# Kernel optimization log

Hardware: AMD Instinct MI355X
Metric: run time of the kernel (lower is better)

## Reference

```python
import jax, jax.numpy as jnp
import numpy as np
from jax import lax

THRESH = 1.0
MIN_VMEM = -1.0

def _conv(x, w, stride):
    # x: [N,C,H,W], w: [O,I,kh,kw]
    return lax.conv_general_dilated(
        x, w, window_strides=(stride, stride), padding=((1, 1), (1, 1)),
        dimension_numbers=("NCHW", "OIHW", "NCHW"))

def _avgpool2(x):
    n, c, h, w = x.shape
    return x.reshape(n, c, h // 2, 2, w // 2, 2).mean(axis=(3, 5))

def _iaf(x_bt, B, T):
    # x_bt: [B*T, ...] -> sinabs IAFSqueeze: reshape to [B,T,...], scan over T.
    feat = x_bt.shape[1:]
    seq = x_bt.reshape((B, T) + feat)
    seq_t = jnp.moveaxis(seq, 1, 0)  # [T, B, ...]

    def step(v, u):
        v = v + u                              # integrate
        s = (v >= THRESH).astype(v.dtype)      # SingleSpike
        v = v * (1.0 - s)                      # MembraneReset -> 0
        v = jnp.maximum(v, MIN_VMEM)           # min_v_mem clamp
        return v, s

    v0 = jnp.zeros(seq_t.shape[1:], dtype=x_bt.dtype)
    _, spikes = lax.scan(step, v0, seq_t)      # spikes: [T, B, ...]
    return jnp.moveaxis(spikes, 0, 1).reshape((B * T,) + feat)

def setup_inputs() -> dict:
    key = jax.random.key(0)
    k0, k1, k2, k3, k4 = jax.random.split(key, 5)
    x = jax.random.normal(k0, (25, 40, 2, 128, 128), jnp.float32)
    w1 = jax.random.normal(k1, (8, 2, 3, 3), jnp.float32) * 0.3
    w2 = jax.random.normal(k2, (16, 8, 3, 3), jnp.float32) * 0.2
    w3 = jax.random.normal(k3, (64, 1024), jnp.float32) * 0.1
    w4 = jax.random.normal(k4, (11, 64), jnp.float32) * 0.2
    return {"x": x, "w1": w1, "w2": w2, "w3": w3, "w4": w4}

def reference(x, w1, w2, w3, w4):
    B, T, C, H, W = x.shape
    h = x.reshape(B * T, C, H, W)
    h = _conv(h, w1, 2)          # [BT, 8, 64, 64]
    h = _iaf(h, B, T)
    h = _avgpool2(h)             # [BT, 8, 32, 32]
    h = _conv(h, w2, 2)          # [BT, 16, 16, 16]
    h = _iaf(h, B, T)
    h = _avgpool2(h)             # [BT, 16, 8, 8]
    h = h.reshape(B * T, -1)     # [BT, 1024]
    h = h @ w3.T                 # [BT, 64]
    h = _iaf(h, B, T)
    h = h @ w4.T                 # [BT, 11]
    h = _iaf(h, B, T)
    return h.reshape(B, T, -1)
```

## Files before the change

### kernel.cpp

```cpp
#include <hip/hip_runtime.h>

#define THRESH 1.0f
#define MIN_VMEM -1.0f

__device__ __forceinline__ float iaf_step(float& v, float u) {
    v += u;
    float s = (v >= THRESH) ? 1.f : 0.f;
    v = (s > 0.f) ? 0.f : v;
    v = fmaxf(v, MIN_VMEM);
    return s;
}

#define K1_CIS 612

__global__ __launch_bounds__(64) void k1_conv1_iaf_pool(
        const float* __restrict__ x, const float* __restrict__ w1,
        float* __restrict__ ws1) {
    __shared__ float B[2][2 * K1_CIS];
    const int tid = threadIdx.x;
    const int cg = tid >> 5;
    const int pp = tid & 31;
    const int px = pp & 7, py = pp >> 3;
    const int tx = blockIdx.x & 3;
    const int ty = blockIdx.x >> 2;
    const int b = blockIdx.y;

    float w[72];
    {
        const float4* wp = (const float4*)(w1 + cg * 72);
        #pragma unroll
        for (int i = 0; i < 18; i++) {
            float4 t4 = wp[i];
            w[4 * i] = t4.x; w[4 * i + 1] = t4.y;
            w[4 * i + 2] = t4.z; w[4 * i + 3] = t4.w;
        }
    }

    int fo[5]; bool lv[5]; int lo[5];
    #pragma unroll
    for (int k = 0; k < 5; k++) {
        const int i = tid + 64 * k;
        const int ci = (i >= 136) ? 1 : 0;
        const int rr = i - 136 * ci;
        const int r = rr >> 3, c4 = rr & 7;
        const int gy = 16 * ty - 1 + r;
        fo[k] = ci * 16384 + gy * 128 + 32 * tx + 4 * c4;
        lv[k] = (gy >= 0) && (i < 272);
        lo[k] = ci * K1_CIS + r * 36 + 1 + 4 * c4;
    }
    const int hci = (tid >= 17) ? 1 : 0;
    const int hr = tid - 17 * hci;
    const int hgy = 16 * ty - 1 + hr;
    const int hfo = hci * 16384 + hgy * 128 + 32 * tx - 1;
    const bool hv_ok = (tid < 34) && (tx > 0) && (hgy >= 0);
    const int hlo = hci * K1_CIS + hr * 36;

    float v[16], u[16];
    #pragma unroll
    for (int i = 0; i < 16; i++) v[i] = 0.f;

    const float* xb = x + (size_t)(b * 40) * 32768;
    float4 rv[5]; float hvv;

    #pragma unroll
    for (int k = 0; k < 5; k++)
        rv[k] = lv[k] ? *(const float4*)(xb + fo[k]) : make_float4(0, 0, 0, 0);
    hvv = hv_ok ? xb[hfo] : 0.f;
    #pragma unroll
    for (int k = 0; k < 4; k++) {
        float* d = &B[0][lo[k]];
        d[0] = rv[k].x; d[1] = rv[k].y; d[2] = rv[k].z; d[3] = rv[k].w;
    }
    if (tid < 16) {
        float* d = &B[0][lo[4]];
        d[0] = rv[4].x; d[1] = rv[4].y; d[2] = rv[4].z; d[3] = rv[4].w;
    }
    if (tid < 34) B[0][hlo] = hvv;

    for (int t = 0; t < 40; t++) {
        const int cur = t & 1;
        if (t < 39) {
            const float* xt = xb + (size_t)(t + 1) * 32768;
            #pragma unroll
            for (int k = 0; k < 5; k++)
                rv[k] = lv[k] ? *(const float4*)(xt + fo[k]) : make_float4(0, 0, 0, 0);
            hvv = hv_ok ? xt[hfo] : 0.f;
        }
        #pragma unroll
        for (int i = 0; i < 16; i++) u[i] = 0.f;
        const float* Bc = B[cur];
        #pragma unroll
        for (int ci = 0; ci < 2; ci++) {
            float p[5][5];
            const int base = ci * K1_CIS + 4 * py * 36 + 4 * px;
            #pragma unroll
            for (int dy = 0; dy < 5; dy++) {
                const float4 q = *(const float4*)&Bc[base + dy * 36];
                p[dy][0] = q.x; p[dy][1] = q.y; p[dy][2] = q.z; p[dy][3] = q.w;
                p[dy][4] = Bc[base + dy * 36 + 4];
            }
            #pragma unroll
            for (int j = 0; j < 4; j++)
                #pragma unroll
                for (int sy = 0; sy < 2; sy++)
                    #pragma unroll
                    for (int sx = 0; sx < 2; sx++) {
                        float a = u[j * 4 + 2 * sy + sx];
                        #pragma unroll
                        for (int ky = 0; ky < 3; ky++)
                            #pragma unroll
                            for (int kx = 0; kx < 3; kx++)
                                a += p[2 * sy + ky][2 * sx + kx]
                                   * w[j * 18 + ci * 9 + ky * 3 + kx];
                        u[j * 4 + 2 * sy + sx] = a;
                    }
        }
        const size_t ob = (size_t)(b * 40 + t) * 8192
                        + (size_t)(4 * ty + py) * 32 + 8 * tx + px;
        #pragma unroll
        for (int j = 0; j < 4; j++) {
            float s = 0.f;
            #pragma unroll
            for (int s4 = 0; s4 < 4; s4++)
                s += iaf_step(v[j * 4 + s4], u[j * 4 + s4]);
            ws1[ob + (size_t)(4 * cg + j) * 1024] = s * 0.25f;
        }
        if (t < 39) {
            float* Bn = B[1 - cur];
            #pragma unroll
            for (int k = 0; k < 4; k++) {
                float* d = &Bn[lo[k]];
                d[0] = rv[k].x; d[1] = rv[k].y; d[2] = rv[k].z; d[3] = rv[k].w;
            }
            if (tid < 16) {
                float* d = &Bn[lo[4]];
                d[0] = rv[4].x; d[1] = rv[4].y; d[2] = rv[4].z; d[3] = rv[4].w;
            }
            if (tid < 34) Bn[hlo] = hvv;
        }
    }
}

#define K2_CIS 1224

__global__ __launch_bounds__(256) void k2a_conv2(
        const float* __restrict__ ws1, const float* __restrict__ w2,
        float* __restrict__ u2) {
    __shared__ float F[8 * K2_CIS];
    const int n = blockIdx.x;
    const int tid = threadIdx.x;

    for (int i = tid; i < 8 * K2_CIS; i += 256) F[i] = 0.f;
    __syncthreads();
    const float4* src = (const float4*)(ws1 + (size_t)n * 8192);
    #pragma unroll
    for (int k = 0; k < 8; k++) {
        const int i = tid + 256 * k;
        const float4 q = src[i];
        const int ci = i >> 8;
        const int rr = i & 255;
        const int r = rr >> 3, c4 = rr & 7;
        float* d = &F[ci * K2_CIS + (r + 1) * 36 + 1 + 4 * c4];
        d[0] = q.x; d[1] = q.y; d[2] = q.z; d[3] = q.w;
    }
    __syncthreads();

    const int wv = tid >> 6;
    const int ln = tid & 63;
    const int oy = ln >> 2;
    const int ox4 = ln & 3;

    float acc[4][4];
    #pragma unroll
    for (int j = 0; j < 4; j++)
        #pragma unroll
        for (int k = 0; k < 4; k++) acc[j][k] = 0.f;

    #pragma unroll
    for (int ci = 0; ci < 8; ci++) {
        float q[3][9];
        const int base = ci * K2_CIS + (2 * oy) * 36 + 8 * ox4;
        #pragma unroll
        for (int ky = 0; ky < 3; ky++) {
            const float4 qa = *(const float4*)&F[base + ky * 36];
            const float4 qb = *(const float4*)&F[base + ky * 36 + 4];
            q[ky][0] = qa.x; q[ky][1] = qa.y; q[ky][2] = qa.z; q[ky][3] = qa.w;
            q[ky][4] = qb.x; q[ky][5] = qb.y; q[ky][6] = qb.z; q[ky][7] = qb.w;
            q[ky][8] = F[base + ky * 36 + 8];
        }
        #pragma unroll
        for (int j = 0; j < 4; j++) {
            const int co_u = __builtin_amdgcn_readfirstlane(4 * wv + j);
            const float* wb = w2 + co_u * 72 + ci * 9;
            float wm[9];
            #pragma unroll
            for (int m = 0; m < 9; m++) wm[m] = wb[m];
            #pragma unroll
            for (int k = 0; k < 4; k++)
                #pragma unroll
                for (int ky = 0; ky < 3; ky++)
                    #pragma unroll
                    for (int kx = 0; kx < 3; kx++)
                        acc[j][k] += q[ky][2 * k + kx] * wm[ky * 3 + kx];
        }
    }
    float* db = u2 + (size_t)n * 4096 + oy * 16 + 4 * ox4;
    #pragma unroll
    for (int j = 0; j < 4; j++) {
        const int co = 4 * wv + j;
        *(float4*)(db + co * 256) =
            make_float4(acc[j][0], acc[j][1], acc[j][2], acc[j][3]);
    }
}

__global__ __launch_bounds__(256) void k2b_scan(
        const float* __restrict__ u2, float* __restrict__ ws2) {
    const int id = blockIdx.x * 256 + threadIdx.x;
    const int b = id >> 10;
    const int c = (id >> 6) & 15;
    const int pp = id & 63;
    const int py = pp >> 3, px = pp & 7;
    const float* base = u2 + (size_t)(b * 40) * 4096 + c * 256
                      + (2 * py) * 16 + 2 * px;
    float* ob = ws2 + (size_t)(b * 40) * 1024 + c * 64 + py * 8 + px;

    float v0 = 0.f, v1 = 0.f, v2 = 0.f, v3 = 0.f;
    float2 P[2][8][2];
    #pragma unroll
    for (int tt = 0; tt < 8; tt++) {
        const float* nb = base + (size_t)tt * 4096;
        P[0][tt][0] = *(const float2*)(nb);
        P[0][tt][1] = *(const float2*)(nb + 16);
    }
    #pragma unroll
    for (int bt = 0; bt < 5; bt++) {
        if (bt < 4) {
            #pragma unroll
            for (int tt = 0; tt < 8; tt++) {
                const float* nb = base + (size_t)(8 * (bt + 1) + tt) * 4096;
                P[(bt + 1) & 1][tt][0] = *(const float2*)(nb);
                P[(bt + 1) & 1][tt][1] = *(const float2*)(nb + 16);
            }
        }
        #pragma unroll
        for (int tt = 0; tt < 8; tt++) {
            const float2 b0 = P[bt & 1][tt][0];
            const float2 b1 = P[bt & 1][tt][1];
            const float s = iaf_step(v0, b0.x) + iaf_step(v1, b0.y)
                          + iaf_step(v2, b1.x) + iaf_step(v3, b1.y);
            ob[(size_t)(8 * bt + tt) * 1024] = s * 0.25f;
        }
    }
}

__global__ __launch_bounds__(256) void k3_fc1(
        const float* __restrict__ ws2, const float* __restrict__ w3,
        float* __restrict__ ws3) {
    __shared__ float rows[4096];
    const int n0 = blockIdx.x * 4;
    const int tid = threadIdx.x;
    const float4* s = (const float4*)(ws2 + (size_t)n0 * 1024);
    #pragma unroll
    for (int k = 0; k < 4; k++)
        ((float4*)rows)[tid + 256 * k] = s[tid + 256 * k];
    __syncthreads();
    const int o = tid >> 2, ko = tid & 3;
    const float4* wp = (const float4*)(w3 + (size_t)o * 1024 + ko * 256);
    const float4* r0 = (const float4*)(rows + ko * 256);
    const float4* r1 = (const float4*)(rows + 1024 + ko * 256);
    const float4* r2 = (const float4*)(rows + 2048 + ko * 256);
    const float4* r3 = (const float4*)(rows + 3072 + ko * 256);
    float a0 = 0.f, a1 = 0.f, a2 = 0.f, a3 = 0.f;
    #pragma unroll 8
    for (int j = 0; j < 64; j++) {
        const float4 wv = wp[j];
        const float4 q0 = r0[j], q1 = r1[j], q2 = r2[j], q3 = r3[j];
        a0 += q0.x * wv.x + q0.y * wv.y + q0.z * wv.z + q0.w * wv.w;
        a1 += q1.x * wv.x + q1.y * wv.y + q1.z * wv.z + q1.w * wv.w;
        a2 += q2.x * wv.x + q2.y * wv.y + q2.z * wv.z + q2.w * wv.w;
        a3 += q3.x * wv.x + q3.y * wv.y + q3.z * wv.z + q3.w * wv.w;
    }
    a0 += __shfl_xor(a0, 1); a0 += __shfl_xor(a0, 2);
    a1 += __shfl_xor(a1, 1); a1 += __shfl_xor(a1, 2);
    a2 += __shfl_xor(a2, 1); a2 += __shfl_xor(a2, 2);
    a3 += __shfl_xor(a3, 1); a3 += __shfl_xor(a3, 2);
    if (ko == 0) {
        ws3[(size_t)(n0 + 0) * 64 + o] = a0;
        ws3[(size_t)(n0 + 1) * 64 + o] = a1;
        ws3[(size_t)(n0 + 2) * 64 + o] = a2;
        ws3[(size_t)(n0 + 3) * 64 + o] = a3;
    }
}

__global__ __launch_bounds__(64) void k4_iaf_fc2_iaf(
        const float* __restrict__ ws3, const float* __restrict__ w4,
        float* __restrict__ out) {
    __shared__ float sld[40 * 64];
    __shared__ float w4s[11 * 66];
    __shared__ float sp[64];
    const int b = blockIdx.x, tid = threadIdx.x;
    for (int i = tid; i < 2560; i += 64) sld[i] = ws3[(size_t)b * 2560 + i];
    for (int i = tid; i < 704; i += 64) {
        int r = i >> 6, cc = i & 63;
        w4s[r * 66 + cc] = w4[i];
    }
    __syncthreads();
    float v1 = 0.f, v2 = 0.f;
    for (int t = 0; t < 40; t++) {
        sp[tid] = iaf_step(v1, sld[t * 64 + tid]);
        __syncthreads();
        if (tid < 11) {
            float acc = 0.f;
            #pragma unroll
            for (int k = 0; k < 64; k++) acc += sp[k] * w4s[tid * 66 + k];
            out[(size_t)(b * 40 + t) * 11 + tid] = iaf_step(v2, acc);
        }
        __syncthreads();
    }
}

extern "C" void kernel_launch(void* const* d_in, const int* in_sizes, int n_in,
                              void* d_out, int out_size, void* d_ws, size_t ws_size,
                              hipStream_t stream) {
    const float* x  = (const float*)d_in[0];
    const float* w1 = (const float*)d_in[1];
    const float* w2 = (const float*)d_in[2];
    const float* w3 = (const float*)d_in[3];
    const float* w4 = (const float*)d_in[4];
    float* out = (float*)d_out;

    float* ws1 = (float*)d_ws;
    float* ws2 = ws1 + 8192000;
    float* ws3 = ws2 + 1024000;
    float* u2 = (float*)d_in[0];

    k1_conv1_iaf_pool<<<dim3(32, 25), 64, 0, stream>>>(x, w1, ws1);
    k2a_conv2<<<1000, 256, 0, stream>>>(ws1, w2, u2);
    k2b_scan<<<100, 256, 0, stream>>>(u2, ws2);
    k3_fc1<<<250, 256, 0, stream>>>(ws2, w3, ws3);
    k4_iaf_fc2_iaf<<<25, 64, 0, stream>>>(ws3, w4, out);
}
```

Before: 282.1 us.

## Shrink per-block work to raise block counts and parallelize the fc2 stage

The conv1 kernel now covers half the tile width with four channel groups of two channels each, which doubles the grid to 1600 blocks and halves per-thread registers. The k2b scan uses 64-thread blocks (400 blocks) and fc1 handles two rows per block (500 blocks). Both changes aim to fill more CUs. The final fc2 kernel first runs the layer-3 IAF scan for all timesteps, then computes all 440 dot products in parallel, and leaves only the 11-wide final scan serial. This replaces the per-timestep barrier loop. The new code relies on single-wavefront execution rather than explicit barriers around LDS reuse, and conv1 re-reads more halo data per output.

```diff
diff --git a/kernel.cpp b/kernel.cpp
--- a/kernel.cpp
+++ b/kernel.cpp
@@ -11,96 +11,98 @@
     return s;
 }
 
-#define K1_CIS 612
+#define K1_CIS 340
 
 __global__ __launch_bounds__(64) void k1_conv1_iaf_pool(
         const float* __restrict__ x, const float* __restrict__ w1,
         float* __restrict__ ws1) {
     __shared__ float B[2][2 * K1_CIS];
     const int tid = threadIdx.x;
-    const int cg = tid >> 5;
-    const int pp = tid & 31;
-    const int px = pp & 7, py = pp >> 3;
-    const int tx = blockIdx.x & 3;
-    const int ty = blockIdx.x >> 2;
+    const int cg = tid >> 4;
+    const int pp = tid & 15;
+    const int ppx = pp & 3, ppy = pp >> 2;
+    const int tx = blockIdx.x & 7;
+    const int ty = blockIdx.x >> 3;
     const int b = blockIdx.y;
 
-    float w[72];
+    for (int i = tid; i < 4 * K1_CIS; i += 64) ((float*)B)[i] = 0.f;
+
+    float w[36];
     {
-        const float4* wp = (const float4*)(w1 + cg * 72);
-        #pragma unroll
-        for (int i = 0; i < 18; i++) {
-            float4 t4 = wp[i];
-            w[4 * i] = t4.x; w[4 * i + 1] = t4.y;
-            w[4 * i + 2] = t4.z; w[4 * i + 3] = t4.w;
-        }
-    }
-
-    int fo[5]; bool lv[5]; int lo[5];
-    #pragma unroll
-    for (int k = 0; k < 5; k++) {
+        const float4* wp = (const float4*)(w1 + cg * 36);
+        #pragma unroll
+        for (int i = 0; i < 9; i++) {
+            const float4 q = wp[i];
+            w[4 * i] = q.x; w[4 * i + 1] = q.y;
+            w[4 * i + 2] = q.z; w[4 * i + 3] = q.w;
+        }
+    }
+
+    int fo[3], lo[3]; bool lv[3];
+    #pragma unroll
+    for (int k = 0; k < 3; k++) {
         const int i = tid + 64 * k;
-        const int ci = (i >= 136) ? 1 : 0;
-        const int rr = i - 136 * ci;
-        const int r = rr >> 3, c4 = rr & 7;
+        const int ci = (i >= 68) ? 1 : 0;
+        const int rr = i - 68 * ci;
+        const int r = rr >> 2, c4 = rr & 3;
         const int gy = 16 * ty - 1 + r;
-        fo[k] = ci * 16384 + gy * 128 + 32 * tx + 4 * c4;
-        lv[k] = (gy >= 0) && (i < 272);
-        lo[k] = ci * K1_CIS + r * 36 + 1 + 4 * c4;
+        fo[k] = ci * 16384 + gy * 128 + 16 * tx + 4 * c4;
+        lv[k] = (i < 136) && (gy >= 0);
+        lo[k] = ci * K1_CIS + r * 20 + 1 + 4 * c4;
     }
     const int hci = (tid >= 17) ? 1 : 0;
     const int hr = tid - 17 * hci;
     const int hgy = 16 * ty - 1 + hr;
-    const int hfo = hci * 16384 + hgy * 128 + 32 * tx - 1;
-    const bool hv_ok = (tid < 34) && (tx > 0) && (hgy >= 0);
-    const int hlo = hci * K1_CIS + hr * 36;
-
-    float v[16], u[16];
-    #pragma unroll
-    for (int i = 0; i < 16; i++) v[i] = 0.f;
+    const int hfo = hci * 16384 + hgy * 128 + 16 * tx - 1;
+    const bool hok = (tid < 34) && (tx > 0) && (hgy >= 0);
+    const int hlo = hci * K1_CIS + hr * 20;
+
+    float v[8];
+    #pragma unroll
+    for (int i = 0; i < 8; i++) v[i] = 0.f;
 
     const float* xb = x + (size_t)(b * 40) * 32768;
-    float4 rv[5]; float hvv;
-
-    #pragma unroll
-    for (int k = 0; k < 5; k++)
+    float4 rv[3]; float hvv;
+
+    #pragma unroll
+    for (int k = 0; k < 3; k++)
         rv[k] = lv[k] ? *(const float4*)(xb + fo[k]) : make_float4(0, 0, 0, 0);
-    hvv = hv_ok ? xb[hfo] : 0.f;
-    #pragma unroll
-    for (int k = 0; k < 4; k++) {
-        float* d = &B[0][lo[k]];
-        d[0] = rv[k].x; d[1] = rv[k].y; d[2] = rv[k].z; d[3] = rv[k].w;
-    }
-    if (tid < 16) {
-        float* d = &B[0][lo[4]];
-        d[0] = rv[4].x; d[1] = rv[4].y; d[2] = rv[4].z; d[3] = rv[4].w;
-    }
+    hvv = hok ? xb[hfo] : 0.f;
+    #pragma unroll
+    for (int k = 0; k < 3; k++)
+        if (tid + 64 * k < 136) {
+            float* d = &B[0][lo[k]];
+            d[0] = rv[k].x; d[1] = rv[k].y; d[2] = rv[k].z; d[3] = rv[k].w;
+        }
     if (tid < 34) B[0][hlo] = hvv;
+
+    const int pyg = 4 * ty + ppy, pxg = 4 * tx + ppx;
 
     for (int t = 0; t < 40; t++) {
         const int cur = t & 1;
         if (t < 39) {
             const float* xt = xb + (size_t)(t + 1) * 32768;
             #pragma unroll
-            for (int k = 0; k < 5; k++)
+            for (int k = 0; k < 3; k++)
                 rv[k] = lv[k] ? *(const float4*)(xt + fo[k]) : make_float4(0, 0, 0, 0);
-            hvv = hv_ok ? xt[hfo] : 0.f;
-        }
-        #pragma unroll
-        for (int i = 0; i < 16; i++) u[i] = 0.f;
+            hvv = hok ? xt[hfo] : 0.f;
+        }
+        float u[8];
+        #pragma unroll
+        for (int i = 0; i < 8; i++) u[i] = 0.f;
         const float* Bc = B[cur];
         #pragma unroll
         for (int ci = 0; ci < 2; ci++) {
             float p[5][5];
-            const int base = ci * K1_CIS + 4 * py * 36 + 4 * px;
+            const int base = ci * K1_CIS + 4 * ppy * 20 + 4 * ppx;
             #pragma unroll
             for (int dy = 0; dy < 5; dy++) {
-                const float4 q = *(const float4*)&Bc[base + dy * 36];
+                const float4 q = *(const float4*)&Bc[base + dy * 20];
                 p[dy][0] = q.x; p[dy][1] = q.y; p[dy][2] = q.z; p[dy][3] = q.w;
-                p[dy][4] = Bc[base + dy * 36 + 4];
+                p[dy][4] = Bc[base + dy * 20 + 4];
             }
             #pragma unroll
-            for (int j = 0; j < 4; j++)
+            for (int j = 0; j < 2; j++)
                 #pragma unroll
                 for (int sy = 0; sy < 2; sy++)
                     #pragma unroll
@@ -115,27 +117,23 @@
                         u[j * 4 + 2 * sy + sx] = a;
                     }
         }
-        const size_t ob = (size_t)(b * 40 + t) * 8192
-                        + (size_t)(4 * ty + py) * 32 + 8 * tx + px;
-        #pragma unroll
-        for (int j = 0; j < 4; j++) {
+        const size_t ob = (size_t)(b * 40 + t) * 8192 + pyg * 32 + pxg;
+        #pragma unroll
+        for (int j = 0; j < 2; j++) {
             float s = 0.f;
             #pragma unroll
             for (int s4 = 0; s4 < 4; s4++)
                 s += iaf_step(v[j * 4 + s4], u[j * 4 + s4]);
-            ws1[ob + (size_t)(4 * cg + j) * 1024] = s * 0.25f;
+            ws1[ob + (size_t)(2 * cg + j) * 1024] = s * 0.25f;
         }
         if (t < 39) {
             float* Bn = B[1 - cur];
             #pragma unroll
-            for (int k = 0; k < 4; k++) {
-                float* d = &Bn[lo[k]];
-                d[0] = rv[k].x; d[1] = rv[k].y; d[2] = rv[k].z; d[3] = rv[k].w;
-            }
-            if (tid < 16) {
-                float* d = &Bn[lo[4]];
-                d[0] = rv[4].x; d[1] = rv[4].y; d[2] = rv[4].z; d[3] = rv[4].w;
-            }
+            for (int k = 0; k < 3; k++)
+                if (tid + 64 * k < 136) {
+                    float* d = &Bn[lo[k]];
+                    d[0] = rv[k].x; d[1] = rv[k].y; d[2] = rv[k].z; d[3] = rv[k].w;
+                }
             if (tid < 34) Bn[hlo] = hvv;
         }
     }
@@ -213,9 +211,9 @@
     }
 }
 
-__global__ __launch_bounds__(256) void k2b_scan(
+__global__ __launch_bounds__(64) void k2b_scan(
         const float* __restrict__ u2, float* __restrict__ ws2) {
-    const int id = blockIdx.x * 256 + threadIdx.x;
+    const int id = blockIdx.x * 64 + threadIdx.x;
     const int b = id >> 10;
     const int c = (id >> 6) & 15;
     const int pp = id & 63;
@@ -256,66 +254,74 @@
 __global__ __launch_bounds__(256) void k3_fc1(
         const float* __restrict__ ws2, const float* __restrict__ w3,
         float* __restrict__ ws3) {
-    __shared__ float rows[4096];
-    const int n0 = blockIdx.x * 4;
+    __shared__ float rows[2048];
+    const int n0 = blockIdx.x * 2;
     const int tid = threadIdx.x;
     const float4* s = (const float4*)(ws2 + (size_t)n0 * 1024);
     #pragma unroll
-    for (int k = 0; k < 4; k++)
+    for (int k = 0; k < 2; k++)
         ((float4*)rows)[tid + 256 * k] = s[tid + 256 * k];
     __syncthreads();
     const int o = tid >> 2, ko = tid & 3;
     const float4* wp = (const float4*)(w3 + (size_t)o * 1024 + ko * 256);
     const float4* r0 = (const float4*)(rows + ko * 256);
     const float4* r1 = (const float4*)(rows + 1024 + ko * 256);
-    const float4* r2 = (const float4*)(rows + 2048 + ko * 256);
-    const float4* r3 = (const float4*)(rows + 3072 + ko * 256);
-    float a0 = 0.f, a1 = 0.f, a2 = 0.f, a3 = 0.f;
+    float a0 = 0.f, a1 = 0.f;
     #pragma unroll 8
     for (int j = 0; j < 64; j++) {
         const float4 wv = wp[j];
-        const float4 q0 = r0[j], q1 = r1[j], q2 = r2[j], q3 = r3[j];
+        const float4 q0 = r0[j], q1 = r1[j];
         a0 += q0.x * wv.x + q0.y * wv.y + q0.z * wv.z + q0.w * wv.w;
         a1 += q1.x * wv.x + q1.y * wv.y + q1.z * wv.z + q1.w * wv.w;
-        a2 += q2.x * wv.x + q2.y * wv.y + q2.z * wv.z + q2.w * wv.w;
-        a3 += q3.x * wv.x + q3.y * wv.y + q3.z * wv.z + q3.w * wv.w;
     }
     a0 += __shfl_xor(a0, 1); a0 += __shfl_xor(a0, 2);
     a1 += __shfl_xor(a1, 1); a1 += __shfl_xor(a1, 2);
-    a2 += __shfl_xor(a2, 1); a2 += __shfl_xor(a2, 2);
-    a3 += __shfl_xor(a3, 1); a3 += __shfl_xor(a3, 2);
     if (ko == 0) {
         ws3[(size_t)(n0 + 0) * 64 + o] = a0;
         ws3[(size_t)(n0 + 1) * 64 + o] = a1;
-        ws3[(size_t)(n0 + 2) * 64 + o] = a2;
-        ws3[(size_t)(n0 + 3) * 64 + o] = a3;
     }
 }
 
 __global__ __launch_bounds__(64) void k4_iaf_fc2_iaf(
         const float* __restrict__ ws3, const float* __restrict__ w4,
         float* __restrict__ out) {
-    __shared__ float sld[40 * 64];
-    __shared__ float w4s[11 * 66];
-    __shared__ float sp[64];
+    __shared__ float sp[40 * 64];
+    __shared__ float pre[40 * 12];
+    __shared__ float w4s[704];
     const int b = blockIdx.x, tid = threadIdx.x;
-    for (int i = tid; i < 2560; i += 64) sld[i] = ws3[(size_t)b * 2560 + i];
-    for (int i = tid; i < 704; i += 64) {
-        int r = i >> 6, cc = i & 63;
-        w4s[r * 66 + cc] = w4[i];
-    }
-    __syncthreads();
-    float v1 = 0.f, v2 = 0.f;
-    for (int t = 0; t < 40; t++) {
-        sp[tid] = iaf_step(v1, sld[t * 64 + tid]);
-        __syncthreads();
-        if (tid < 11) {
+
+    #pragma unroll
+    for (int i = 0; i < 3; i++) {
+        const int k = tid + 64 * i;
+        if (k < 176) ((float4*)w4s)[k] = ((const float4*)w4)[k];
+    }
+    {
+        float v1 = 0.f;
+        const float* src = ws3 + (size_t)b * 2560 + tid;
+        #pragma unroll
+        for (int t = 0; t < 40; t++)
+            sp[t * 64 + tid] = iaf_step(v1, src[t * 64]);
+    }
+    #pragma unroll
+    for (int r2 = 0; r2 < 7; r2++) {
+        const int idx = tid + 64 * r2;
+        if (idx < 440) {
+            const int t = idx % 40, o = idx / 40;
+            const float4* spr = (const float4*)(sp + t * 64);
+            const float4* wr = (const float4*)(w4s + o * 64);
             float acc = 0.f;
             #pragma unroll
-            for (int k = 0; k < 64; k++) acc += sp[k] * w4s[tid * 66 + k];
-            out[(size_t)(b * 40 + t) * 11 + tid] = iaf_step(v2, acc);
-        }
-        __syncthreads();
+            for (int q = 0; q < 16; q++) {
+                const float4 a = spr[q], ww = wr[q];
+                acc += a.x * ww.x + a.y * ww.y + a.z * ww.z + a.w * ww.w;
+            }
+            pre[t * 12 + o] = acc;
+        }
+    }
+    if (tid < 11) {
+        float v2 = 0.f;
+        for (int t = 0; t < 40; t++)
+            out[(size_t)(b * 40 + t) * 11 + tid] = iaf_step(v2, pre[t * 12 + tid]);
     }
 }
 
@@ -334,9 +340,9 @@
     float* ws3 = ws2 + 1024000;
     float* u2 = (float*)d_in[0];
 
-    k1_conv1_iaf_pool<<<dim3(32, 25), 64, 0, stream>>>(x, w1, ws1);
+    k1_conv1_iaf_pool<<<dim3(64, 25), 64, 0, stream>>>(x, w1, ws1);
     k2a_conv2<<<1000, 256, 0, stream>>>(ws1, w2, u2);
-    k2b_scan<<<100, 256, 0, stream>>>(u2, ws2);
-    k3_fc1<<<250, 256, 0, stream>>>(ws2, w3, ws3);
+    k2b_scan<<<400, 64, 0, stream>>>(u2, ws2);
+    k3_fc1<<<500, 256, 0, stream>>>(ws2, w3, ws3);
     k4_iaf_fc2_iaf<<<25, 64, 0, stream>>>(ws3, w4, out);
 }
```

Result: no change. 285.2 us (+1.1%).
